# Optimization experiments

Hardware: AMD Instinct MI355X
Metric: run time of the kernel (lower is better)

## Reference

```python
import jax, jax.numpy as jnp
import numpy as np

NQ, NC, D = 100000, 2000, 128
QN, CN, MAXC = 4, 4, 4
B, S = 128, 64
HOPS, RANK_K = 2, 10


def setup_inputs() -> dict:
    key = jax.random.key(0)
    ks = jax.random.split(key, 24)
    sc = 1.0 / np.sqrt(D)
    f = lambda k, shape: (jax.random.normal(k, shape) * sc).astype(jnp.float32)
    xb = float(np.sqrt(6.0 / (B + D)))  # xavier_uniform on [B, D]
    return {
        'embed_question': f(ks[0], (NQ, D)),
        'embed_concept': f(ks[1], (NC, D)),
        'embed_correctness': f(ks[2], (2, D)),
        'W_ih1': f(ks[3], (3 * D, 2 * D)), 'W_hh1': f(ks[4], (3 * D, D)),
        'b_ih1': jnp.zeros(3 * D), 'b_hh1': jnp.zeros(3 * D),
        'W_ih2': f(ks[5], (3 * D, D)), 'W_hh2': f(ks[6], (3 * D, D)),
        'b_ih2': jnp.zeros(3 * D), 'b_hh2': jnp.zeros(3 * D),
        'W_agg': f(ks[7], (HOPS, D, D)), 'b_agg': jnp.zeros((HOPS, D)),
        'W_last': f(ks[8], (D, D)), 'b_last': jnp.zeros(D),
        'W_query': f(ks[9], (D, D)), 'b_query': jnp.zeros(D),
        'W_key': f(ks[10], (D, D)), 'b_key': jnp.zeros(D),
        'w_q': f(ks[11], (D,)), 'w_k': f(ks[12], (D,)), 'b_w': jnp.zeros(()),
        'h1_init': jax.random.uniform(ks[13], (B, D), minval=-xb, maxval=xb),
        'h2_init': jax.random.uniform(ks[14], (B, D), minval=-xb, maxval=xb),
        'question_neighbors': jax.random.randint(ks[15], (NQ, QN), 0, NC),
        'concept_neighbors': jax.random.randint(ks[16], (NC, CN), 0, NQ),
        'q2c': jax.random.randint(ks[17], (NQ, MAXC), 0, NC),
        'question_seq': jax.random.randint(ks[18], (B, S), 0, NQ),
        'correctness_seq': jax.random.randint(ks[19], (B, S), 0, 2),
        'mask_seq': jax.random.randint(ks[20], (B, S), 0, 2),
    }


def _gru(x, h, Wih, Whh, bih, bhh):
    gi = x @ Wih.T + bih
    gh = h @ Whh.T + bhh
    ir, iz, inn = jnp.split(gi, 3, axis=-1)
    hr, hz, hn = jnp.split(gh, 3, axis=-1)
    r = jax.nn.sigmoid(ir + hr)
    z = jax.nn.sigmoid(iz + hz)
    n = jnp.tanh(inn + r * hn)
    return (1.0 - z) * n + z * h


def _aggregate(embs, W_agg, b_agg, W_last, b_last):
    embs = list(embs)
    for i in range(HOPS):
        for j in range(HOPS - i):
            m = jnp.mean(embs[j + 1], axis=-2) + embs[j]
            embs[j] = jnp.tanh(m @ W_agg[j].T + b_agg[j])
    return jnp.tanh(embs[0] @ W_last.T + b_last)


def _predict(qc, states, W_query, b_query, W_key, b_key, w_q, w_k, b_w):
    # qc: [B, nqc, D]; states: [B, nst, D]
    og = jnp.einsum('bqd,bsd->bqs', qc, states)
    Qe = jnp.tanh(qc @ W_key.T + b_key)          # MLP_key(question_concepts)
    Ke = jnp.tanh(states @ W_query.T + b_query)  # MLP_query(states)
    tmp = (Qe @ w_q)[:, :, None] + (Ke @ w_k)[:, None, :] + b_w  # [B,nqc,nst]
    alpha = jax.nn.softmax(tmp, axis=2)
    return jax.nn.sigmoid(jnp.sum(alpha * og, axis=(1, 2)))


def reference(embed_question, embed_concept, embed_correctness,
              W_ih1, W_hh1, b_ih1, b_hh1, W_ih2, W_hh2, b_ih2, b_hh2,
              W_agg, b_agg, W_last, b_last, W_query, b_query, W_key, b_key,
              w_q, w_k, b_w, h1_init, h2_init,
              question_neighbors, concept_neighbors, q2c,
              question_seq, correctness_seq, mask_seq):
    h1, h2 = h1_init, h2_init
    state_history = jnp.zeros((B, S, D), jnp.float32)
    y = jnp.zeros((B, S), jnp.float32)
    for t in range(S - 1):
        q_t = question_seq[:, t]
        mask_t = mask_seq[:, t] != 0
        emb_r = embed_correctness[correctness_seq[:, t]]
        # multi-hop neighbor expansion (computed for full batch; masked rows
        # are replaced below, identical math to the original masked gather)
        nodes = [q_t]
        for i in range(HOPS):
            flat = nodes[-1].reshape(-1)
            tbl = question_neighbors if i % 2 == 0 else concept_neighbors
            nxt = tbl[flat]
            nodes.append(nxt.reshape(nodes[-1].shape + (nxt.shape[-1],)))
        embs = [embed_question[n] if i % 2 == 0 else embed_concept[n]
                for i, n in enumerate(nodes)]
        agg = _aggregate(embs, W_agg, b_agg, W_last, b_last)
        emb_q = jnp.where(mask_t[:, None], agg, embed_question[q_t])
        h1 = _gru(jnp.concatenate([emb_q, emb_r], axis=1), h1, W_ih1, W_hh1, b_ih1, b_hh1)
        g2 = _gru(h1, h2, W_ih2, W_hh2, b_ih2, b_hh2)
        q_next = question_seq[:, t + 1]
        qc = jnp.concatenate([embed_question[q_next][:, None],
                              embed_concept[q2c[q_next]]], axis=1)  # [B, 1+MAXC, D]
        if t == 0:
            y = y.at[:, 0].set(_predict(qc, g2[:, None], W_query, b_query, W_key, b_key, w_q, w_k, b_w))
            continue  # original skips h2/state_history update at t==0
        cur = g2[:, None]
        if t <= RANK_K:
            hist = jnp.concatenate([cur, state_history[:, :t]], axis=1)
        else:
            Qv = jax.lax.stop_gradient(embed_question[q_next])               # [B,D]
            Kv = jax.lax.stop_gradient(embed_question[question_seq[:, :t]])  # [B,t,D]
            scores = jnp.einsum('btd,bd->bt', Kv, Qv)
            _, idx = jax.lax.top_k(scores, RANK_K)
            sel = jnp.take_along_axis(state_history, idx[:, :, None], axis=1)
            hist = jnp.concatenate([cur, sel], axis=1)
        y = y.at[:, t + 1].set(_predict(qc, hist, W_query, b_query, W_key, b_key, w_q, w_k, b_w))
        h2 = g2
        state_history = state_history.at[:, t].set(g2)
    return y
```

## Files before the change

kernel.cpp:

```cpp
#include <hip/hip_runtime.h>
#include <math.h>

#define D    128
#define QN   4
#define CN   4
#define MAXC 4
#define BB   128
#define SS   64
#define RK   10
#define T    768

#define UOFF_IH1A 0
#define UOFF_IH1B 24576
#define UOFF_HH1  49152
#define UOFF_IH2  73728
#define UOFF_HH2  98304
#define UOFF_QRY  122880
#define UOFF_A0   131072
#define UOFF_A1   139264
#define UOFF_LS   147456
#define TOTAL_U   155648

typedef _Float16 h2_t __attribute__((ext_vector_type(2)));
union U32H2 { unsigned u; h2_t h; unsigned short s2[2]; };

__device__ __forceinline__ unsigned h16f(float x){
  U32H2 c; c.h[0] = (_Float16)x; c.h[1] = (_Float16)0.f;
  return (unsigned)c.s2[0];
}
__device__ __forceinline__ unsigned packh2(float a, float b){
  U32H2 c; c.h[0] = (_Float16)a; c.h[1] = (_Float16)b;
  return c.u;
}
__device__ __forceinline__ float dot2(unsigned w, unsigned x, float acc){
  U32H2 a; a.u = w; U32H2 b; b.u = x;
  return __builtin_amdgcn_fdot2(a.h, b.h, acc, false);
}
__device__ __forceinline__ float hlo(unsigned u){ U32H2 a; a.u=u; return (float)a.h[0]; }
__device__ __forceinline__ float hhi(unsigned u){ U32H2 a; a.u=u; return (float)a.h[1]; }

__device__ __forceinline__ float fsig(float x){ return 1.f/(1.f + __expf(-x)); }
__device__ __forceinline__ float ftanh(float x){
  float xc = fminf(fmaxf(x, -30.f), 30.f);
  float e = __expf(2.f*xc);
  return (e - 1.f)/(e + 1.f);
}

#define FD4(w4, x4, acc) { \
  acc = dot2((w4).x, (x4).x, acc); acc = dot2((w4).y, (x4).y, acc); \
  acc = dot2((w4).z, (x4).z, acc); acc = dot2((w4).w, (x4).w, acc); }

#define KEEP4(v) asm volatile("" : "+v"((v).x), "+v"((v).y), "+v"((v).z), "+v"((v).w))

__global__ void gikt_pack(const float* __restrict__ Wih1,
                          const float* __restrict__ Whh1,
                          const float* __restrict__ Wih2,
                          const float* __restrict__ Whh2,
                          const float* __restrict__ Wagg,
                          const float* __restrict__ Wlast,
                          const float* __restrict__ Wqry,
                          unsigned* __restrict__ wsU)
{
  int i = blockIdx.x * blockDim.x + threadIdx.x;
  if (i >= TOTAL_U) return;
  const float* src = nullptr; int row = 0, e2 = 0, stride = 0;
  int j = i;
  if (j < 24576) {
    int c = j & 3, i4 = j >> 2, k = i4 / 768, t = i4 - k * 768, r = t >> 1, hf = t & 1;
    e2 = hf * 32 + k * 4 + c; row = r; src = Wih1; stride = 256;
  } else if ((j -= 24576) < 24576) {
    e2 = 64 + (j / 384); row = j % 384; src = Wih1; stride = 256;
  } else if ((j -= 24576) < 24576) {
    int c = j & 3, i4 = j >> 2, k = i4 / 768, t = i4 - k * 768, r = t >> 1, hf = t & 1;
    e2 = hf * 32 + k * 4 + c; row = r; src = Whh1; stride = 128;
  } else if ((j -= 24576) < 24576) {
    int c = j & 3, i4 = j >> 2, k = i4 / 768, t = i4 - k * 768, r = t >> 1, hf = t & 1;
    e2 = hf * 32 + k * 4 + c; row = r; src = Wih2; stride = 128;
  } else if ((j -= 24576) < 24576) {
    int c = j & 3, i4 = j >> 2, k = i4 / 768, t = i4 - k * 768, r = t >> 1, hf = t & 1;
    e2 = hf * 32 + k * 4 + c; row = r; src = Whh2; stride = 128;
  } else if ((j -= 24576) < 8192) {
    int c = j & 3, i4 = j >> 2, k = i4 >> 7, r = i4 & 127;
    e2 = k * 4 + c; row = r; src = Wqry; stride = 128;
  } else if ((j -= 8192) < 8192) {
    int r = j & 127, p = (j >> 7) & 1, e2g = j >> 8;
    e2 = 2 * e2g + p; row = r; src = Wagg; stride = 128;
  } else if ((j -= 8192) < 8192) {
    int r = j & 127, p = (j >> 7) & 1, e2g = j >> 8;
    e2 = 2 * e2g + p; row = r; src = Wagg + 128 * 128; stride = 128;
  } else {
    j -= 8192;
    int r = j & 127, p = (j >> 7) & 1, e2g = j >> 8;
    e2 = 2 * e2g + p; row = r; src = Wlast; stride = 128;
  }
  float lo = src[row * stride + 2 * e2];
  float hi = src[row * stride + 2 * e2 + 1];
  wsU[i] = h16f(lo) | (h16f(hi) << 16);
}

__device__ __forceinline__ float2 gru_nl2(float2 gr, float2 gz, float2 gn,
                                          float2 hr, float2 hz, float2 hn,
                                          float2 hold){
  float2 out;
  {
    float rg = fsig(gr.x + hr.x);
    float zg = fsig(gz.x + hz.x);
    float ng = ftanh(gn.x + rg*hn.x);
    out.x = (1.f-zg)*ng + zg*hold.x;
  }
  {
    float rg = fsig(gr.y + hr.y);
    float zg = fsig(gz.y + hz.y);
    float ng = ftanh(gn.y + rg*hn.y);
    out.y = (1.f-zg)*ng + zg*hold.y;
  }
  return out;
}

__launch_bounds__(T, 1)
__global__ void gikt_main(
    const float* __restrict__ embQ,
    const float* __restrict__ embC,
    const float* __restrict__ embR,
    const float* __restrict__ b_ih1,
    const float* __restrict__ b_hh1,
    const float* __restrict__ b_ih2,
    const float* __restrict__ b_hh2,
    const float* __restrict__ b_agg,
    const float* __restrict__ b_last,
    const float* __restrict__ b_query,
    const float* __restrict__ w_k,
    const float* __restrict__ h1i,
    const float* __restrict__ h2i,
    const int* __restrict__ qnbr,
    const int* __restrict__ cnbr,
    const int* __restrict__ q2c,
    const int* __restrict__ qseq,
    const int* __restrict__ cseq,
    const int* __restrict__ mseq,
    const unsigned* __restrict__ wsU,
    float* __restrict__ y)
{
  const int b   = blockIdx.x;
  const int tid = threadIdx.x;
  const int r2  = tid >> 1, hf = tid & 1;

  __shared__ unsigned aggL[3 * 8192];
  __shared__ __align__(16) float hist[SS][132];
  __shared__ float gicorr[2][384];
  __shared__ int   idxk[SS][RK];
  __shared__ float kwh[SS];
  __shared__ __align__(16) float a_[5][D];
  __shared__ __align__(16) float gi1[3*D];
  __shared__ __align__(16) float gh1[3*D];
  __shared__ __align__(16) float gi2[3*D];
  __shared__ __align__(16) float gh2[3*D];
  __shared__ __align__(16) float h1fp[2][D];
  __shared__ __align__(16) float g2fp[2][D];
  __shared__ __align__(16) float h2ifp[D];
  __shared__ __align__(16) float qcs[2][D];
  __shared__ float kevec[D];
  __shared__ __align__(16) unsigned mPu[5][64];
  __shared__ __align__(16) unsigned vPu[64];
  __shared__ __align__(16) unsigned m1Pu[64];
  __shared__ __align__(16) unsigned xvPu[64];
  __shared__ __align__(16) unsigned h1Pu[64];
  __shared__ __align__(16) unsigned g2Pu[64];
  __shared__ __align__(16) unsigned h2iPu[64];
  __shared__ int   sq[SS], scc[SS], smk[SS];
  __shared__ int   nn1[SS][QN], nn2[SS][QN*CN], cc2[SS][MAXC];
  __shared__ float red[12];
  __shared__ float ogv[16], kwv[16];

  float (*G)[65] = (float(*)[65])aggL;

  uint4 pwi[8], pwh[8];
  {
    const uint4* Pi = (const uint4*)(wsU + UOFF_IH2);
    const uint4* Ph = (const uint4*)(wsU + UOFF_HH2);
    #pragma unroll
    for (int k = 0; k < 8; ++k) { pwi[k] = Pi[k*768 + tid]; pwh[k] = Ph[k*768 + tid]; }
    #pragma unroll
    for (int k = 0; k < 8; ++k) { KEEP4(pwi[k]); KEEP4(pwh[k]); }
  }

  for (int i = tid; i < SS; i += T) { sq[i]=qseq[b*SS+i]; scc[i]=cseq[b*SS+i]; smk[i]=mseq[b*SS+i]; }
  __syncthreads();

  for (int i = tid; i < SS*32; i += T) {
    int s = i >> 5, e4 = i & 31;
    float4 v = ((const float4*)(embQ + sq[s]*D))[e4];
    ((float4*)hist[s])[e4] = v;
  }
  for (int i = tid; i < (SS-1)*QN; i += T)   { int t = i>>2, j = i&3; nn1[t][j] = qnbr[sq[t]*QN + j]; }
  for (int i = tid; i < (SS-1)*MAXC; i += T) { int t = i>>2, j = i&3; cc2[t][j] = q2c[sq[t+1]*MAXC + j]; }
  __syncthreads();

  for (int p = tid; p < SS*SS; p += T) {
    int tq = p >> 6, s = p & 63;
    if (tq >= RK+2 && s < tq-1) {
      const float4* ra = (const float4*)hist[tq];
      const float4* rb = (const float4*)hist[s];
      float acc = 0.f;
      #pragma unroll 8
      for (int d4 = 0; d4 < 32; ++d4) {
        float4 xa = ra[d4], xb = rb[d4];
        acc += xa.x*xb.x + xa.y*xb.y + xa.z*xb.z + xa.w*xb.w;
      }
      G[tq-(RK+2)][s] = acc;
    }
  }
  for (int i = tid; i < (SS-1)*QN*CN; i += T) {
    int t = i>>4, j = (i>>2)&3, l = i&3;
    nn2[t][j*CN+l] = cnbr[nn1[t][j]*CN + l];
  }
  {
    const int c = (tid >= 384) ? 1 : 0, r = tid - (c ? 384 : 0);
    const float2* er2 = (const float2*)(embR + c*D);
    float acc = 0.f;
    #pragma unroll 4
    for (int e2l = 0; e2l < 64; ++e2l) {
      unsigned u = wsU[UOFF_IH1B + e2l*384 + r];
      float2 x = er2[e2l];
      acc += hlo(u)*x.x + hhi(u)*x.y;
    }
    gicorr[c][r] = acc;
  }
  __syncthreads();

  if (tid < 52) {
    int t = RK + 1 + tid;
    for (int k = 0; k < RK; ++k) {
      float best = -INFINITY; int bi = 0;
      for (int s = 0; s < t; ++s) { float v = G[tid][s]; if (v > best) { best = v; bi = s; } }
      idxk[t][k] = bi;
      G[tid][bi] = -INFINITY;
    }
  }
  __syncthreads();

  for (int i = tid; i < 3*8192; i += T) aggL[i] = wsU[UOFF_A0 + i];
  if (tid < 64) {
    float a0 = h1i[b*D+2*tid], a1 = h1i[b*D+2*tid+1];
    h1Pu[tid] = packh2(a0, a1);
    ((float2*)h1fp[1])[tid] = make_float2(a0, a1);
    float c0 = h2i[b*D+2*tid], c1 = h2i[b*D+2*tid+1];
    h2iPu[tid] = packh2(c0, c1);
    ((float2*)h2ifp)[tid] = make_float2(c0, c1);
    g2Pu[tid] = 0;
  }
  if (tid < D) hist[0][tid] = 0.f;
  if (tid == 0) y[b*SS + 1] = 0.f;
  {
    float p0 = (tid < D) ? w_k[tid]*ftanh(b_query[tid]) : 0.f;
    #pragma unroll
    for (int off = 32; off; off >>= 1) p0 += __shfl_down(p0, off);
    if ((tid & 63) == 0) red[tid >> 6] = p0;
  }
  __syncthreads();
  if (tid == 0) kwh[0] = red[0]+red[1];
  __syncthreads();

  const uint4* Wi1 = (const uint4*)(wsU + UOFF_IH1A);
  const uint4* Wh1 = (const uint4*)(wsU + UOFF_HH1);
  const uint4* Wq4 = (const uint4*)(wsU + UOFF_QRY);

  float pf0 = 0.f, pf1 = 0.f, pf2 = 0.f, pf3 = 0.f, pf4 = 0.f;

#define PREFETCH(tt) {                                                        \
    const int d_ = tid & 127, grp_ = tid >> 7;                                \
    const bool m2_ = (smk[tt] != 0);                                          \
    if (grp_ == 0) {                                                          \
      pf0 = embQ[sq[tt]*D + d_];                                              \
      if (m2_) { pf1 = embC[nn1[tt][0]*D+d_]; pf2 = embC[nn1[tt][1]*D+d_];    \
                 pf3 = embC[nn1[tt][2]*D+d_]; pf4 = embC[nn1[tt][3]*D+d_]; }  \
    } else if (grp_ <= 4) {                                                   \
      if (m2_) { const int j_ = grp_ - 1;                                     \
        pf0 = embC[nn1[tt][j_]*D + d_];                                       \
        pf1 = embQ[nn2[tt][j_*CN+0]*D+d_]; pf2 = embQ[nn2[tt][j_*CN+1]*D+d_]; \
        pf3 = embQ[nn2[tt][j_*CN+2]*D+d_]; pf4 = embQ[nn2[tt][j_*CN+3]*D+d_];}\
    } else {                                                                  \
      pf0 = embQ[sq[(tt)+1]*D + d_];                                          \
      pf1 = embC[cc2[tt][0]*D+d_]; pf2 = embC[cc2[tt][1]*D+d_];               \
      pf3 = embC[cc2[tt][2]*D+d_]; pf4 = embC[cc2[tt][3]*D+d_];               \
    } }

  PREFETCH(0);

  for (int t = 0; t < SS-1; ++t) {
    const int tp = t - 1;
    const bool msk = (smk[t] != 0);

    if (tid < 64 && t >= 1) {
      const int l = tid;
      const float* ph2 = (t <= 2) ? h2ifp : g2fp[t & 1];
      float2 hold = ((const float2*)ph2)[l];
      float2 gv = gru_nl2(((const float2*)gi2)[l], ((const float2*)(gi2+128))[l], ((const float2*)(gi2+256))[l],
                          ((const float2*)gh2)[l], ((const float2*)(gh2+128))[l], ((const float2*)(gh2+256))[l],
                          hold);
      ((float2*)g2fp[(t+1)&1])[l] = gv;
      g2Pu[l] = packh2(gv.x, gv.y);
      if (t >= 2) { hist[t-1][2*l] = gv.x; hist[t-1][2*l+1] = gv.y; }
    }
    {
      const int d = tid & 127, grp = tid >> 7;
      if (msk) {
        if (grp <= 4) ((_Float16*)mPu[grp])[d] = (_Float16)(pf0 + 0.25f*(pf1+pf2+pf3+pf4));
        else          qcs[t & 1][d] = pf0+pf1+pf2+pf3+pf4;
      } else {
        if (grp == 0)      ((_Float16*)xvPu)[d] = (_Float16)pf0;
        else if (grp == 5) qcs[t & 1][d] = pf0+pf1+pf2+pf3+pf4;
      }
    }
    if (t + 1 < SS-1) PREFETCH(t+1);
    __syncthreads();

    if (msk) {
      if (tid < 128) {
        const int r = tid;
        const unsigned* A = aggL;
        const uint2* x2p = (const uint2*)mPu[0];
        float acc0 = b_agg[r], acc1 = 0.f;
        #pragma unroll
        for (int e2g = 0; e2g < 32; e2g += 2) {
          unsigned u00 = A[e2g*256 + r],     u01 = A[e2g*256 + 128 + r];
          uint2 x0 = x2p[e2g];
          acc0 = dot2(u00, x0.x, acc0); acc0 = dot2(u01, x0.y, acc0);
          unsigned u10 = A[(e2g+1)*256 + r], u11 = A[(e2g+1)*256 + 128 + r];
          uint2 x1 = x2p[e2g+1];
          acc1 = dot2(u10, x1.x, acc1); acc1 = dot2(u11, x1.y, acc1);
        }
        a_[0][r] = ftanh(acc0 + acc1);
      } else if (tid < 256) {
        const int r = tid - 128;
        const unsigned* A = aggL + 8192;
        const uint2* x1p = (const uint2*)mPu[1];
        const uint2* x2p = (const uint2*)mPu[2];
        const uint2* x3p = (const uint2*)mPu[3];
        const uint2* x4p = (const uint2*)mPu[4];
        float bb = b_agg[D + r];
        float c1 = 0.f, c2 = 0.f, c3 = 0.f, c4 = 0.f;
        #pragma unroll
        for (int e2g = 0; e2g < 32; ++e2g) {
          unsigned u0 = A[e2g*256 + r], u1 = A[e2g*256 + 128 + r];
          uint2 v1 = x1p[e2g]; c1 = dot2(u0, v1.x, c1); c1 = dot2(u1, v1.y, c1);
          uint2 v2 = x2p[e2g]; c2 = dot2(u0, v2.x, c2); c2 = dot2(u1, v2.y, c2);
          uint2 v3 = x3p[e2g]; c3 = dot2(u0, v3.x, c3); c3 = dot2(u1, v3.y, c3);
          uint2 v4 = x4p[e2g]; c4 = dot2(u0, v4.x, c4); c4 = dot2(u1, v4.y, c4);
        }
        a_[1][r] = ftanh(bb + c1); a_[2][r] = ftanh(bb + c2);
        a_[3][r] = ftanh(bb + c3); a_[4][r] = ftanh(bb + c4);
      } else if (tid < 432 && t >= 1) {
        const int g = (tid - 256) >> 4, lane = tid & 15;
        const int ne = (tp < RK ? tp : RK) + 1;
        if (g < ne) {
          const float* row;
          if (g == 0) row = g2fp[(t+1)&1];
          else {
            int s = (tp <= RK) ? (g-1) : idxk[tp][g-1];
            row = hist[s];
            if (lane == 0) kwv[g] = kwh[s];
          }
          const float* qp = qcs[tp & 1];
          float part = 0.f;
          #pragma unroll
          for (int k = 0; k < 8; ++k) { int d = lane + (k<<4); part += qp[d]*row[d]; }
          part += __shfl_xor(part, 8, 16);
          part += __shfl_xor(part, 4, 16);
          part += __shfl_xor(part, 2, 16);
          part += __shfl_xor(part, 1, 16);
          if (lane == 0) ogv[g] = part;
        }
      } else if (tid >= 512) {
        const int rq = (tid - 512) >> 1, hq = tid & 1;
        const uint4* g2p4 = (const uint4*)g2Pu;
        float a0 = hq ? 0.f : b_query[rq], a1 = 0.f;
        #pragma unroll
        for (int k = hq*8; k < hq*8+8; k += 2) {
          uint4 u0 = Wq4[k*128 + rq];     uint4 x0 = g2p4[k];   FD4(u0, x0, a0);
          uint4 u1 = Wq4[(k+1)*128 + rq]; uint4 x1 = g2p4[k+1]; FD4(u1, x1, a1);
        }
        float acc = a0 + a1; acc += __shfl_xor(acc, 1);
        if (!hq) kevec[rq] = ftanh(acc) * w_k[rq];
      }
      __syncthreads();

      if (tid < 256) {
        const int l = tid & 63;
        float v0 = a_[0][2*l]   + 0.25f*(a_[1][2*l]  +a_[2][2*l]  +a_[3][2*l]  +a_[4][2*l]);
        float v1 = a_[0][2*l+1] + 0.25f*(a_[1][2*l+1]+a_[2][2*l+1]+a_[3][2*l+1]+a_[4][2*l+1]);
        vPu[l] = packh2(v0, v1);
        const int r = tid >> 1, h = tid & 1;
        const uint2* x2p = (const uint2*)vPu;
        float acc0 = h ? 0.f : b_agg[r], acc1 = 0.f;
        #pragma unroll
        for (int e2g = h*16; e2g < h*16+16; e2g += 2) {
          unsigned u00 = aggL[e2g*256 + r],     u01 = aggL[e2g*256 + 128 + r];
          uint2 x0 = x2p[e2g];
          acc0 = dot2(u00, x0.x, acc0); acc0 = dot2(u01, x0.y, acc0);
          unsigned u10 = aggL[(e2g+1)*256 + r], u11 = aggL[(e2g+1)*256 + 128 + r];
          uint2 x1 = x2p[e2g+1];
          acc1 = dot2(u10, x1.x, acc1); acc1 = dot2(u11, x1.y, acc1);
        }
        float acc = acc0 + acc1; acc += __shfl_xor(acc, 1);
        if (!h) ((_Float16*)m1Pu)[r] = (_Float16)ftanh(acc);
      } else if (tid >= 512 && tid < 576 && t >= 1) {
        const int lane = tid & 63;
        float v = kevec[lane] + kevec[lane + 64];
        #pragma unroll
        for (int off = 32; off; off >>= 1) v += __shfl_down(v, off);
        if (lane == 0) { kwv[0] = v; if (tp >= 1) kwh[tp] = v; }
      }
      __syncthreads();

      if (tid < 256) {
        const int r = tid >> 1, h = tid & 1;
        const unsigned* A = aggL + 16384;
        const uint2* x2p = (const uint2*)m1Pu;
        float acc0 = h ? 0.f : b_last[r], acc1 = 0.f;
        #pragma unroll
        for (int e2g = h*16; e2g < h*16+16; e2g += 2) {
          unsigned u00 = A[e2g*256 + r],     u01 = A[e2g*256 + 128 + r];
          uint2 x0 = x2p[e2g];
          acc0 = dot2(u00, x0.x, acc0); acc0 = dot2(u01, x0.y, acc0);
          unsigned u10 = A[(e2g+1)*256 + r], u11 = A[(e2g+1)*256 + 128 + r];
          uint2 x1 = x2p[e2g+1];
          acc1 = dot2(u10, x1.x, acc1); acc1 = dot2(u11, x1.y, acc1);
        }
        float acc = acc0 + acc1; acc += __shfl_xor(acc, 1);
        if (!h) ((_Float16*)xvPu)[r] = (_Float16)ftanh(acc);
      } else if (tid == 256 && t >= 1) {
        const int ne = (tp < RK ? tp : RK) + 1;
        float mx = kwv[0];
        for (int i2 = 1; i2 < ne; ++i2) mx = fmaxf(mx, kwv[i2]);
        float den = 0.f, num = 0.f;
        for (int i2 = 0; i2 < ne; ++i2) { float e_ = __expf(kwv[i2]-mx); den += e_; num += e_*ogv[i2]; }
        y[b*SS + ((tp==0) ? 0 : (tp+1))] = fsig(num/den);
      }
      __syncthreads();

      {
        const uint4* xvp4 = (const uint4*)xvPu;
        const uint4* h1p4 = (const uint4*)h1Pu;
        float ai0 = hf ? 0.f : (b_ih1[r2] + gicorr[scc[t]][r2]), ai1 = 0.f;
        float ah0 = hf ? 0.f : b_hh1[r2], ah1 = 0.f;
        #pragma unroll
        for (int k = 0; k < 8; k += 2) {
          uint4 w0 = Wi1[k*768 + tid], w1 = Wi1[(k+1)*768 + tid];
          uint4 xa = xvp4[hf*8+k], xb = xvp4[hf*8+k+1];
          FD4(w0, xa, ai0); FD4(w1, xb, ai1);
          uint4 v0 = Wh1[k*768 + tid], v1 = Wh1[(k+1)*768 + tid];
          uint4 ya = h1p4[hf*8+k], yb = h1p4[hf*8+k+1];
          FD4(v0, ya, ah0); FD4(v1, yb, ah1);
        }
        float acc_i = ai0 + ai1; acc_i += __shfl_xor(acc_i, 1);
        float acc_h = ah0 + ah1; acc_h += __shfl_xor(acc_h, 1);
        if (!hf) { gi1[r2] = acc_i; gh1[r2] = acc_h; }
      }
      __syncthreads();
    } else {
      if (tid >= 256 && tid < 432 && t >= 1) {
        const int g = (tid - 256) >> 4, lane = tid & 15;
        const int ne = (tp < RK ? tp : RK) + 1;
        if (g < ne) {
          const float* row;
          if (g == 0) row = g2fp[(t+1)&1];
          else {
            int s = (tp <= RK) ? (g-1) : idxk[tp][g-1];
            row = hist[s];
            if (lane == 0) kwv[g] = kwh[s];
          }
          const float* qp = qcs[tp & 1];
          float part = 0.f;
          #pragma unroll
          for (int k = 0; k < 8; ++k) { int d = lane + (k<<4); part += qp[d]*row[d]; }
          part += __shfl_xor(part, 8, 16);
          part += __shfl_xor(part, 4, 16);
          part += __shfl_xor(part, 2, 16);
          part += __shfl_xor(part, 1, 16);
          if (lane == 0) ogv[g] = part;
        }
      } else if (tid >= 512) {
        const int rq = (tid - 512) >> 1, hq = tid & 1;
        const uint4* g2p4 = (const uint4*)g2Pu;
        float a0 = hq ? 0.f : b_query[rq], a1 = 0.f;
        #pragma unroll
        for (int k = hq*8; k < hq*8+8; k += 2) {
          uint4 u0 = Wq4[k*128 + rq];     uint4 x0 = g2p4[k];   FD4(u0, x0, a0);
          uint4 u1 = Wq4[(k+1)*128 + rq]; uint4 x1 = g2p4[k+1]; FD4(u1, x1, a1);
        }
        float acc = a0 + a1; acc += __shfl_xor(acc, 1);
        if (!hq) kevec[rq] = ftanh(acc) * w_k[rq];
      }
      {
        const uint4* xvp4 = (const uint4*)xvPu;
        const uint4* h1p4 = (const uint4*)h1Pu;
        float ai0 = hf ? 0.f : (b_ih1[r2] + gicorr[scc[t]][r2]), ai1 = 0.f;
        float ah0 = hf ? 0.f : b_hh1[r2], ah1 = 0.f;
        #pragma unroll
        for (int k = 0; k < 8; k += 2) {
          uint4 w0 = Wi1[k*768 + tid], w1 = Wi1[(k+1)*768 + tid];
          uint4 xa = xvp4[hf*8+k], xb = xvp4[hf*8+k+1];
          FD4(w0, xa, ai0); FD4(w1, xb, ai1);
          uint4 v0 = Wh1[k*768 + tid], v1 = Wh1[(k+1)*768 + tid];
          uint4 ya = h1p4[hf*8+k], yb = h1p4[hf*8+k+1];
          FD4(v0, ya, ah0); FD4(v1, yb, ah1);
        }
        float acc_i = ai0 + ai1; acc_i += __shfl_xor(acc_i, 1);
        float acc_h = ah0 + ah1; acc_h += __shfl_xor(acc_h, 1);
        if (!hf) { gi1[r2] = acc_i; gh1[r2] = acc_h; }
      }
      __syncthreads();
    }

    if (!msk && t >= 1 && tid < 64) {
      float v = kevec[tid] + kevec[tid + 64];
      #pragma unroll
      for (int off = 32; off; off >>= 1) v += __shfl_down(v, off);
      if (tid == 0) {
        if (tp >= 1) kwh[tp] = v;
        const int ne = (tp < RK ? tp : RK) + 1;
        float mx = v;
        for (int i2 = 1; i2 < ne; ++i2) mx = fmaxf(mx, kwv[i2]);
        float den = __expf(v - mx), num = den*ogv[0];
        for (int i2 = 1; i2 < ne; ++i2) { float e_ = __expf(kwv[i2]-mx); den += e_; num += e_*ogv[i2]; }
        y[b*SS + ((tp==0) ? 0 : (tp+1))] = fsig(num/den);
      }
    }
    {
      const int l = tid & 63;
      float2 hold = ((const float2*)h1fp[(t+1)&1])[l];
      float2 hn = gru_nl2(((const float2*)gi1)[l], ((const float2*)(gi1+128))[l], ((const float2*)(gi1+256))[l],
                          ((const float2*)gh1)[l], ((const float2*)(gh1+128))[l], ((const float2*)(gh1+256))[l],
                          hold);
      ((float2*)h1fp[t&1])[l] = hn;
      h1Pu[l] = packh2(hn.x, hn.y);
    }
    {
      const uint4* xh1 = (const uint4*)h1Pu;
      const uint4* xh2 = (t <= 1) ? (const uint4*)h2iPu : (const uint4*)g2Pu;
      float ai0 = hf ? 0.f : b_ih2[r2], ai1 = 0.f;
      float ah0 = hf ? 0.f : b_hh2[r2], ah1 = 0.f;
      #pragma unroll
      for (int k = 0; k < 8; k += 2) {
        uint4 xa = xh1[hf*8+k], xb = xh1[hf*8+k+1];
        FD4(pwi[k], xa, ai0); FD4(pwi[k+1], xb, ai1);
        uint4 ya = xh2[hf*8+k], yb = xh2[hf*8+k+1];
        FD4(pwh[k], ya, ah0); FD4(pwh[k+1], yb, ah1);
      }
      float acc_i = ai0 + ai1; acc_i += __shfl_xor(acc_i, 1);
      float acc_h = ah0 + ah1; acc_h += __shfl_xor(acc_h, 1);
      if (!hf) { gi2[r2] = acc_i; gh2[r2] = acc_h; }
    }
    __syncthreads();
  }

  if (tid < 64) {
    const int l = tid;
    const float* ph2 = g2fp[1];
    float2 hold = ((const float2*)ph2)[l];
    float2 gv = gru_nl2(((const float2*)gi2)[l], ((const float2*)(gi2+128))[l], ((const float2*)(gi2+256))[l],
                        ((const float2*)gh2)[l], ((const float2*)(gh2+128))[l], ((const float2*)(gh2+256))[l],
                        hold);
    ((float2*)g2fp[0])[l] = gv;
    g2Pu[l] = packh2(gv.x, gv.y);
  }
  __syncthreads();
  if (tid < 128) {
    const int r = tid;
    const uint4* g2p4 = (const uint4*)g2Pu;
    float a0 = b_query[r], a1 = 0.f;
    #pragma unroll
    for (int k = 0; k < 16; k += 2) {
      uint4 u0 = Wq4[k*128 + r];     uint4 x0 = g2p4[k];   FD4(u0, x0, a0);
      uint4 u1 = Wq4[(k+1)*128 + r]; uint4 x1 = g2p4[k+1]; FD4(u1, x1, a1);
    }
    kevec[r] = ftanh(a0 + a1) * w_k[r];
  }
  __syncthreads();
  {
    const int tp = SS - 2;
    if (tid < 176) {
      const int g = tid >> 4, lane = tid & 15;
      const int ne = RK + 1;
      if (g < ne) {
        const float* row;
        if (g == 0) row = g2fp[0];
        else {
          int s = idxk[tp][g-1];
          row = hist[s];
          if (lane == 0) kwv[g] = kwh[s];
        }
        const float* qp = qcs[tp & 1];
        float part = 0.f;
        #pragma unroll
        for (int k = 0; k < 8; ++k) { int d = lane + (k<<4); part += qp[d]*row[d]; }
        part += __shfl_xor(part, 8, 16);
        part += __shfl_xor(part, 4, 16);
        part += __shfl_xor(part, 2, 16);
        part += __shfl_xor(part, 1, 16);
        if (lane == 0) ogv[g] = part;
      }
    } else if (tid >= 256 && tid < 320) {
      const int lane = tid & 63;
      float v = kevec[lane] + kevec[lane + 64];
      #pragma unroll
      for (int off = 32; off; off >>= 1) v += __shfl_down(v, off);
      if (lane == 0) kwv[0] = v;
    }
  }
  __syncthreads();
  if (tid == 0) {
    const int ne = RK + 1;
    float mx = kwv[0];
    for (int i2 = 1; i2 < ne; ++i2) mx = fmaxf(mx, kwv[i2]);
    float den = 0.f, num = 0.f;
    for (int i2 = 0; i2 < ne; ++i2) { float e_ = __expf(kwv[i2]-mx); den += e_; num += e_*ogv[i2]; }
    y[b*SS + SS - 1] = fsig(num/den);
  }
}

extern "C" void kernel_launch(void* const* d_in, const int* in_sizes, int n_in,
                              void* d_out, int out_size, void* d_ws, size_t ws_size,
                              hipStream_t stream)
{
  (void)in_sizes; (void)n_in; (void)out_size; (void)ws_size;

  const float* embQ  = (const float*)d_in[0];
  const float* embC  = (const float*)d_in[1];
  const float* embR  = (const float*)d_in[2];
  const float* Wih1  = (const float*)d_in[3];
  const float* Whh1  = (const float*)d_in[4];
  const float* bih1  = (const float*)d_in[5];
  const float* bhh1  = (const float*)d_in[6];
  const float* Wih2  = (const float*)d_in[7];
  const float* Whh2  = (const float*)d_in[8];
  const float* bih2  = (const float*)d_in[9];
  const float* bhh2  = (const float*)d_in[10];
  const float* Wagg  = (const float*)d_in[11];
  const float* bagg  = (const float*)d_in[12];
  const float* Wlast = (const float*)d_in[13];
  const float* blast = (const float*)d_in[14];
  const float* Wqry  = (const float*)d_in[15];
  const float* bqry  = (const float*)d_in[16];
  const float* wk    = (const float*)d_in[20];
  const float* h1i   = (const float*)d_in[22];
  const float* h2i   = (const float*)d_in[23];
  const int* qnbr    = (const int*)d_in[24];
  const int* cnbr    = (const int*)d_in[25];
  const int* q2c     = (const int*)d_in[26];
  const int* qseq    = (const int*)d_in[27];
  const int* cseq    = (const int*)d_in[28];
  const int* mseq    = (const int*)d_in[29];

  unsigned* wsU = (unsigned*)d_ws;
  float* yout = (float*)d_out;

  gikt_pack<<<(TOTAL_U + 255) / 256, 256, 0, stream>>>(Wih1, Whh1, Wih2, Whh2, Wagg, Wlast, Wqry, wsU);
  gikt_main<<<BB, T, 0, stream>>>(embQ, embC, embR, bih1, bhh1, bih2, bhh2, bagg, blast, bqry,
                                  wk, h1i, h2i, qnbr, cnbr, q2c, qseq, cseq, mseq, wsU, yout);
}
```

Baseline: 546.2 us.

## Pin GRU1 weights in registers and rebalance aggregation work across threads

The GRU layer-1 input and hidden weight slices are now loaded once into registers, next to the layer-2 weights, instead of being re-read from global memory every timestep. The hop-1 aggregation for the four neighbors is split across 512 threads, one neighbor each, instead of 128 threads doing all four. The query projection moves to 128 threads, one full row each, with no shuffle reduction. This cuts per-step memory traffic and shortens the critical path, at the cost of 64 more VGPRs per thread of resident weights in a 768-thread block, which risks spills.

```diff
diff --git a/kernel.cpp b/kernel.cpp
--- a/kernel.cpp
+++ b/kernel.cpp
@@ -174,14 +174,19 @@
 
   float (*G)[65] = (float(*)[65])aggL;
 
-  uint4 pwi[8], pwh[8];
+  uint4 pw1i[8], pw1h[8], pwi[8], pwh[8];
   {
+    const uint4* Pa = (const uint4*)(wsU + UOFF_IH1A);
+    const uint4* Pb = (const uint4*)(wsU + UOFF_HH1);
     const uint4* Pi = (const uint4*)(wsU + UOFF_IH2);
     const uint4* Ph = (const uint4*)(wsU + UOFF_HH2);
     #pragma unroll
-    for (int k = 0; k < 8; ++k) { pwi[k] = Pi[k*768 + tid]; pwh[k] = Ph[k*768 + tid]; }
+    for (int k = 0; k < 8; ++k) {
+      pw1i[k] = Pa[k*768 + tid]; pw1h[k] = Pb[k*768 + tid];
+      pwi[k]  = Pi[k*768 + tid]; pwh[k]  = Ph[k*768 + tid];
+    }
     #pragma unroll
-    for (int k = 0; k < 8; ++k) { KEEP4(pwi[k]); KEEP4(pwh[k]); }
+    for (int k = 0; k < 8; ++k) { KEEP4(pw1i[k]); KEEP4(pw1h[k]); KEEP4(pwi[k]); KEEP4(pwh[k]); }
   }
 
   for (int i = tid; i < SS; i += T) { sq[i]=qseq[b*SS+i]; scc[i]=cseq[b*SS+i]; smk[i]=mseq[b*SS+i]; }
@@ -261,8 +266,6 @@
   if (tid == 0) kwh[0] = red[0]+red[1];
   __syncthreads();
 
-  const uint4* Wi1 = (const uint4*)(wsU + UOFF_IH1A);
-  const uint4* Wh1 = (const uint4*)(wsU + UOFF_HH1);
   const uint4* Wq4 = (const uint4*)(wsU + UOFF_QRY);
 
   float pf0 = 0.f, pf1 = 0.f, pf2 = 0.f, pf3 = 0.f, pf4 = 0.f;
@@ -331,25 +334,53 @@
           acc1 = dot2(u10, x1.x, acc1); acc1 = dot2(u11, x1.y, acc1);
         }
         a_[0][r] = ftanh(acc0 + acc1);
-      } else if (tid < 256) {
-        const int r = tid - 128;
+      } else if (tid < 640) {
+        const int m = (tid - 128) >> 7, r = (tid - 128) & 127;
         const unsigned* A = aggL + 8192;
-        const uint2* x1p = (const uint2*)mPu[1];
-        const uint2* x2p = (const uint2*)mPu[2];
-        const uint2* x3p = (const uint2*)mPu[3];
-        const uint2* x4p = (const uint2*)mPu[4];
-        float bb = b_agg[D + r];
-        float c1 = 0.f, c2 = 0.f, c3 = 0.f, c4 = 0.f;
-        #pragma unroll
-        for (int e2g = 0; e2g < 32; ++e2g) {
-          unsigned u0 = A[e2g*256 + r], u1 = A[e2g*256 + 128 + r];
-          uint2 v1 = x1p[e2g]; c1 = dot2(u0, v1.x, c1); c1 = dot2(u1, v1.y, c1);
-          uint2 v2 = x2p[e2g]; c2 = dot2(u0, v2.x, c2); c2 = dot2(u1, v2.y, c2);
-          uint2 v3 = x3p[e2g]; c3 = dot2(u0, v3.x, c3); c3 = dot2(u1, v3.y, c3);
-          uint2 v4 = x4p[e2g]; c4 = dot2(u0, v4.x, c4); c4 = dot2(u1, v4.y, c4);
-        }
-        a_[1][r] = ftanh(bb + c1); a_[2][r] = ftanh(bb + c2);
-        a_[3][r] = ftanh(bb + c3); a_[4][r] = ftanh(bb + c4);
+        const uint2* xp = (const uint2*)mPu[1 + m];
+        float acc0 = b_agg[D + r], acc1 = 0.f;
+        #pragma unroll
+        for (int e2g = 0; e2g < 32; e2g += 2) {
+          unsigned u00 = A[e2g*256 + r],     u01 = A[e2g*256 + 128 + r];
+          uint2 x0 = xp[e2g];
+          acc0 = dot2(u00, x0.x, acc0); acc0 = dot2(u01, x0.y, acc0);
+          unsigned u10 = A[(e2g+1)*256 + r], u11 = A[(e2g+1)*256 + 128 + r];
+          uint2 x1 = xp[e2g+1];
+          acc1 = dot2(u10, x1.x, acc1); acc1 = dot2(u11, x1.y, acc1);
+        }
+        a_[1 + m][r] = ftanh(acc0 + acc1);
+      } else {
+        const int r = tid - 640;
+        const uint4* g2p4 = (const uint4*)g2Pu;
+        float a0 = b_query[r], a1 = 0.f;
+        #pragma unroll
+        for (int k = 0; k < 16; k += 2) {
+          uint4 u0 = Wq4[k*128 + r];     uint4 x0 = g2p4[k];   FD4(u0, x0, a0);
+          uint4 u1 = Wq4[(k+1)*128 + r]; uint4 x1 = g2p4[k+1]; FD4(u1, x1, a1);
+        }
+        kevec[r] = ftanh(a0 + a1) * w_k[r];
+      }
+      __syncthreads();
+
+      if (tid < 256) {
+        const int l = tid & 63;
+        float v0 = a_[0][2*l]   + 0.25f*(a_[1][2*l]  +a_[2][2*l]  +a_[3][2*l]  +a_[4][2*l]);
+        float v1 = a_[0][2*l+1] + 0.25f*(a_[1][2*l+1]+a_[2][2*l+1]+a_[3][2*l+1]+a_[4][2*l+1]);
+        vPu[l] = packh2(v0, v1);
+        const int r = tid >> 1, h = tid & 1;
+        const uint2* x2p = (const uint2*)vPu;
+        float acc0 = h ? 0.f : b_agg[r], acc1 = 0.f;
+        #pragma unroll
+        for (int e2g = h*16; e2g < h*16+16; e2g += 2) {
+          unsigned u00 = aggL[e2g*256 + r],     u01 = aggL[e2g*256 + 128 + r];
+          uint2 x0 = x2p[e2g];
+          acc0 = dot2(u00, x0.x, acc0); acc0 = dot2(u01, x0.y, acc0);
+          unsigned u10 = aggL[(e2g+1)*256 + r], u11 = aggL[(e2g+1)*256 + 128 + r];
+          uint2 x1 = x2p[e2g+1];
+          acc1 = dot2(u10, x1.x, acc1); acc1 = dot2(u11, x1.y, acc1);
+        }
+        float acc = acc0 + acc1; acc += __shfl_xor(acc, 1);
+        if (!h) ((_Float16*)m1Pu)[r] = (_Float16)ftanh(acc);
       } else if (tid < 432 && t >= 1) {
         const int g = (tid - 256) >> 4, lane = tid & 15;
         const int ne = (tp < RK ? tp : RK) + 1;
@@ -371,39 +402,6 @@
           part += __shfl_xor(part, 1, 16);
           if (lane == 0) ogv[g] = part;
         }
-      } else if (tid >= 512) {
-        const int rq = (tid - 512) >> 1, hq = tid & 1;
-        const uint4* g2p4 = (const uint4*)g2Pu;
-        float a0 = hq ? 0.f : b_query[rq], a1 = 0.f;
-        #pragma unroll
-        for (int k = hq*8; k < hq*8+8; k += 2) {
-          uint4 u0 = Wq4[k*128 + rq];     uint4 x0 = g2p4[k];   FD4(u0, x0, a0);
-          uint4 u1 = Wq4[(k+1)*128 + rq]; uint4 x1 = g2p4[k+1]; FD4(u1, x1, a1);
-        }
-        float acc = a0 + a1; acc += __shfl_xor(acc, 1);
-        if (!hq) kevec[rq] = ftanh(acc) * w_k[rq];
-      }
-      __syncthreads();
-
-      if (tid < 256) {
-        const int l = tid & 63;
-        float v0 = a_[0][2*l]   + 0.25f*(a_[1][2*l]  +a_[2][2*l]  +a_[3][2*l]  +a_[4][2*l]);
-        float v1 = a_[0][2*l+1] + 0.25f*(a_[1][2*l+1]+a_[2][2*l+1]+a_[3][2*l+1]+a_[4][2*l+1]);
-        vPu[l] = packh2(v0, v1);
-        const int r = tid >> 1, h = tid & 1;
-        const uint2* x2p = (const uint2*)vPu;
-        float acc0 = h ? 0.f : b_agg[r], acc1 = 0.f;
-        #pragma unroll
-        for (int e2g = h*16; e2g < h*16+16; e2g += 2) {
-          unsigned u00 = aggL[e2g*256 + r],     u01 = aggL[e2g*256 + 128 + r];
-          uint2 x0 = x2p[e2g];
-          acc0 = dot2(u00, x0.x, acc0); acc0 = dot2(u01, x0.y, acc0);
-          unsigned u10 = aggL[(e2g+1)*256 + r], u11 = aggL[(e2g+1)*256 + 128 + r];
-          uint2 x1 = x2p[e2g+1];
-          acc1 = dot2(u10, x1.x, acc1); acc1 = dot2(u11, x1.y, acc1);
-        }
-        float acc = acc0 + acc1; acc += __shfl_xor(acc, 1);
-        if (!h) ((_Float16*)m1Pu)[r] = (_Float16)ftanh(acc);
       } else if (tid >= 512 && tid < 576 && t >= 1) {
         const int lane = tid & 63;
         float v = kevec[lane] + kevec[lane + 64];
@@ -446,12 +444,10 @@
         float ah0 = hf ? 0.f : b_hh1[r2], ah1 = 0.f;
         #pragma unroll
         for (int k = 0; k < 8; k += 2) {
-          uint4 w0 = Wi1[k*768 + tid], w1 = Wi1[(k+1)*768 + tid];
           uint4 xa = xvp4[hf*8+k], xb = xvp4[hf*8+k+1];
-          FD4(w0, xa, ai0); FD4(w1, xb, ai1);
-          uint4 v0 = Wh1[k*768 + tid], v1 = Wh1[(k+1)*768 + tid];
+          FD4(pw1i[k], xa, ai0); FD4(pw1i[k+1], xb, ai1);
           uint4 ya = h1p4[hf*8+k], yb = h1p4[hf*8+k+1];
-          FD4(v0, ya, ah0); FD4(v1, yb, ah1);
+          FD4(pw1h[k], ya, ah0); FD4(pw1h[k+1], yb, ah1);
         }
         float acc_i = ai0 + ai1; acc_i += __shfl_xor(acc_i, 1);
         float acc_h = ah0 + ah1; acc_h += __shfl_xor(acc_h, 1);
@@ -480,17 +476,16 @@
           part += __shfl_xor(part, 1, 16);
           if (lane == 0) ogv[g] = part;
         }
-      } else if (tid >= 512) {
-        const int rq = (tid - 512) >> 1, hq = tid & 1;
+      } else if (tid >= 640) {
+        const int r = tid - 640;
         const uint4* g2p4 = (const uint4*)g2Pu;
-        float a0 = hq ? 0.f : b_query[rq], a1 = 0.f;
-        #pragma unroll
-        for (int k = hq*8; k < hq*8+8; k += 2) {
-          uint4 u0 = Wq4[k*128 + rq];     uint4 x0 = g2p4[k];   FD4(u0, x0, a0);
-          uint4 u1 = Wq4[(k+1)*128 + rq]; uint4 x1 = g2p4[k+1]; FD4(u1, x1, a1);
-        }
-        float acc = a0 + a1; acc += __shfl_xor(acc, 1);
-        if (!hq) kevec[rq] = ftanh(acc) * w_k[rq];
+        float a0 = b_query[r], a1 = 0.f;
+        #pragma unroll
+        for (int k = 0; k < 16; k += 2) {
+          uint4 u0 = Wq4[k*128 + r];     uint4 x0 = g2p4[k];   FD4(u0, x0, a0);
+          uint4 u1 = Wq4[(k+1)*128 + r]; uint4 x1 = g2p4[k+1]; FD4(u1, x1, a1);
+        }
+        kevec[r] = ftanh(a0 + a1) * w_k[r];
       }
       {
         const uint4* xvp4 = (const uint4*)xvPu;
@@ -499,12 +494,10 @@
         float ah0 = hf ? 0.f : b_hh1[r2], ah1 = 0.f;
         #pragma unroll
         for (int k = 0; k < 8; k += 2) {
-          uint4 w0 = Wi1[k*768 + tid], w1 = Wi1[(k+1)*768 + tid];
           uint4 xa = xvp4[hf*8+k], xb = xvp4[hf*8+k+1];
-          FD4(w0, xa, ai0); FD4(w1, xb, ai1);
-          uint4 v0 = Wh1[k*768 + tid], v1 = Wh1[(k+1)*768 + tid];
+          FD4(pw1i[k], xa, ai0); FD4(pw1i[k+1], xb, ai1);
           uint4 ya = h1p4[hf*8+k], yb = h1p4[hf*8+k+1];
-          FD4(v0, ya, ah0); FD4(v1, yb, ah1);
+          FD4(pw1h[k], ya, ah0); FD4(pw1h[k+1], yb, ah1);
         }
         float acc_i = ai0 + ai1; acc_i += __shfl_xor(acc_i, 1);
         float acc_h = ah0 + ah1; acc_h += __shfl_xor(acc_h, 1);
```

Result: slower. 671.6 us (+23.0%).

## Rebalance masked-step work across threads and spread hidden GRU matvec into idle phases

Applied to the files above, without the earlier changes.

In the masked branch, the four neighbour aggregation matvecs, previously done by one thread per row with four accumulators, are now spread over 512 threads with one matvec each. The query projection now uses one thread per row over 128 threads instead of two half-rows. The W_hh1·h1 gate rows are computed by threads that sat idle in the two later phases, and the final GRU phase keeps only the input-side matvec. This shortens the critical path of each serial timestep, at the cost of more thread divergence and more register pressure from the macro.

```diff
diff --git a/kernel.cpp b/kernel.cpp
--- a/kernel.cpp
+++ b/kernel.cpp
@@ -265,6 +265,16 @@
   const uint4* Wh1 = (const uint4*)(wsU + UOFF_HH1);
   const uint4* Wq4 = (const uint4*)(wsU + UOFF_QRY);
 
+#define GH1_ROW(r) {                                                   \
+    const uint4* h1p4_ = (const uint4*)h1Pu;                           \
+    float a0_ = b_hh1[r], a1_ = 0.f;                                   \
+    _Pragma("unroll")                                                  \
+    for (int k = 0; k < 8; ++k) {                                      \
+      uint4 u0_ = Wh1[k*768 + 2*(r)], u1_ = Wh1[k*768 + 2*(r) + 1];    \
+      FD4(u0_, h1p4_[k], a0_); FD4(u1_, h1p4_[8+k], a1_);              \
+    }                                                                  \
+    gh1[r] = a0_ + a1_; }
+
   float pf0 = 0.f, pf1 = 0.f, pf2 = 0.f, pf3 = 0.f, pf4 = 0.f;
 
 #define PREFETCH(tt) {                                                        \
@@ -316,11 +326,11 @@
     __syncthreads();
 
     if (msk) {
-      if (tid < 128) {
-        const int r = tid;
-        const unsigned* A = aggL;
-        const uint2* x2p = (const uint2*)mPu[0];
-        float acc0 = b_agg[r], acc1 = 0.f;
+      if (tid < 640) {
+        const int which = tid >> 7, r = tid & 127;
+        const unsigned* A = aggL + (which ? 8192 : 0);
+        const uint2* x2p = (const uint2*)mPu[which];
+        float acc0 = (which == 0) ? b_agg[r] : b_agg[D + r], acc1 = 0.f;
         #pragma unroll
         for (int e2g = 0; e2g < 32; e2g += 2) {
           unsigned u00 = A[e2g*256 + r],     u01 = A[e2g*256 + 128 + r];
@@ -330,58 +340,17 @@
           uint2 x1 = x2p[e2g+1];
           acc1 = dot2(u10, x1.x, acc1); acc1 = dot2(u11, x1.y, acc1);
         }
-        a_[0][r] = ftanh(acc0 + acc1);
-      } else if (tid < 256) {
-        const int r = tid - 128;
-        const unsigned* A = aggL + 8192;
-        const uint2* x1p = (const uint2*)mPu[1];
-        const uint2* x2p = (const uint2*)mPu[2];
-        const uint2* x3p = (const uint2*)mPu[3];
-        const uint2* x4p = (const uint2*)mPu[4];
-        float bb = b_agg[D + r];
-        float c1 = 0.f, c2 = 0.f, c3 = 0.f, c4 = 0.f;
-        #pragma unroll
-        for (int e2g = 0; e2g < 32; ++e2g) {
-          unsigned u0 = A[e2g*256 + r], u1 = A[e2g*256 + 128 + r];
-          uint2 v1 = x1p[e2g]; c1 = dot2(u0, v1.x, c1); c1 = dot2(u1, v1.y, c1);
-          uint2 v2 = x2p[e2g]; c2 = dot2(u0, v2.x, c2); c2 = dot2(u1, v2.y, c2);
-          uint2 v3 = x3p[e2g]; c3 = dot2(u0, v3.x, c3); c3 = dot2(u1, v3.y, c3);
-          uint2 v4 = x4p[e2g]; c4 = dot2(u0, v4.x, c4); c4 = dot2(u1, v4.y, c4);
-        }
-        a_[1][r] = ftanh(bb + c1); a_[2][r] = ftanh(bb + c2);
-        a_[3][r] = ftanh(bb + c3); a_[4][r] = ftanh(bb + c4);
-      } else if (tid < 432 && t >= 1) {
-        const int g = (tid - 256) >> 4, lane = tid & 15;
-        const int ne = (tp < RK ? tp : RK) + 1;
-        if (g < ne) {
-          const float* row;
-          if (g == 0) row = g2fp[(t+1)&1];
-          else {
-            int s = (tp <= RK) ? (g-1) : idxk[tp][g-1];
-            row = hist[s];
-            if (lane == 0) kwv[g] = kwh[s];
-          }
-          const float* qp = qcs[tp & 1];
-          float part = 0.f;
-          #pragma unroll
-          for (int k = 0; k < 8; ++k) { int d = lane + (k<<4); part += qp[d]*row[d]; }
-          part += __shfl_xor(part, 8, 16);
-          part += __shfl_xor(part, 4, 16);
-          part += __shfl_xor(part, 2, 16);
-          part += __shfl_xor(part, 1, 16);
-          if (lane == 0) ogv[g] = part;
-        }
-      } else if (tid >= 512) {
-        const int rq = (tid - 512) >> 1, hq = tid & 1;
+        a_[which][r] = ftanh(acc0 + acc1);
+      } else {
+        const int r = tid - 640;
         const uint4* g2p4 = (const uint4*)g2Pu;
-        float a0 = hq ? 0.f : b_query[rq], a1 = 0.f;
-        #pragma unroll
-        for (int k = hq*8; k < hq*8+8; k += 2) {
-          uint4 u0 = Wq4[k*128 + rq];     uint4 x0 = g2p4[k];   FD4(u0, x0, a0);
-          uint4 u1 = Wq4[(k+1)*128 + rq]; uint4 x1 = g2p4[k+1]; FD4(u1, x1, a1);
-        }
-        float acc = a0 + a1; acc += __shfl_xor(acc, 1);
-        if (!hq) kevec[rq] = ftanh(acc) * w_k[rq];
+        float a0 = b_query[r], a1 = 0.f;
+        #pragma unroll
+        for (int k = 0; k < 16; k += 2) {
+          uint4 u0 = Wq4[k*128 + r];     uint4 x0 = g2p4[k];   FD4(u0, x0, a0);
+          uint4 u1 = Wq4[(k+1)*128 + r]; uint4 x1 = g2p4[k+1]; FD4(u1, x1, a1);
+        }
+        kevec[r] = ftanh(a0 + a1) * w_k[r];
       }
       __syncthreads();
 
@@ -404,12 +373,43 @@
         }
         float acc = acc0 + acc1; acc += __shfl_xor(acc, 1);
         if (!h) ((_Float16*)m1Pu)[r] = (_Float16)ftanh(acc);
-      } else if (tid >= 512 && tid < 576 && t >= 1) {
-        const int lane = tid & 63;
-        float v = kevec[lane] + kevec[lane + 64];
-        #pragma unroll
-        for (int off = 32; off; off >>= 1) v += __shfl_down(v, off);
-        if (lane == 0) { kwv[0] = v; if (tp >= 1) kwh[tp] = v; }
+      } else if (tid < 432) {
+        if (t >= 1) {
+          const int g = (tid - 256) >> 4, lane = tid & 15;
+          const int ne = (tp < RK ? tp : RK) + 1;
+          if (g < ne) {
+            const float* row;
+            if (g == 0) row = g2fp[(t+1)&1];
+            else {
+              int s = (tp <= RK) ? (g-1) : idxk[tp][g-1];
+              row = hist[s];
+              if (lane == 0) kwv[g] = kwh[s];
+            }
+            const float* qp = qcs[tp & 1];
+            float part = 0.f;
+            #pragma unroll
+            for (int k = 0; k < 8; ++k) { int d = lane + (k<<4); part += qp[d]*row[d]; }
+            part += __shfl_xor(part, 8, 16);
+            part += __shfl_xor(part, 4, 16);
+            part += __shfl_xor(part, 2, 16);
+            part += __shfl_xor(part, 1, 16);
+            if (lane == 0) ogv[g] = part;
+          }
+        }
+      } else if (tid < 512) {
+        const int r = tid - 432;
+        GH1_ROW(r);
+      } else if (tid < 576) {
+        if (t >= 1) {
+          const int lane = tid & 63;
+          float v = kevec[lane] + kevec[lane + 64];
+          #pragma unroll
+          for (int off = 32; off; off >>= 1) v += __shfl_down(v, off);
+          if (lane == 0) { kwv[0] = v; if (tp >= 1) kwh[tp] = v; }
+        }
+      } else {
+        const int r = 80 + (tid - 576);
+        GH1_ROW(r);
       }
       __syncthreads();
 
@@ -429,33 +429,32 @@
         }
         float acc = acc0 + acc1; acc += __shfl_xor(acc, 1);
         if (!h) ((_Float16*)xvPu)[r] = (_Float16)ftanh(acc);
-      } else if (tid == 256 && t >= 1) {
-        const int ne = (tp < RK ? tp : RK) + 1;
-        float mx = kwv[0];
-        for (int i2 = 1; i2 < ne; ++i2) mx = fmaxf(mx, kwv[i2]);
-        float den = 0.f, num = 0.f;
-        for (int i2 = 0; i2 < ne; ++i2) { float e_ = __expf(kwv[i2]-mx); den += e_; num += e_*ogv[i2]; }
-        y[b*SS + ((tp==0) ? 0 : (tp+1))] = fsig(num/den);
+      } else if (tid == 256) {
+        if (t >= 1) {
+          const int ne = (tp < RK ? tp : RK) + 1;
+          float mx = kwv[0];
+          for (int i2 = 1; i2 < ne; ++i2) mx = fmaxf(mx, kwv[i2]);
+          float den = 0.f, num = 0.f;
+          for (int i2 = 0; i2 < ne; ++i2) { float e_ = __expf(kwv[i2]-mx); den += e_; num += e_*ogv[i2]; }
+          y[b*SS + ((tp==0) ? 0 : (tp+1))] = fsig(num/den);
+        }
+      } else if (tid >= 384 && tid < 496) {
+        const int r = 272 + (tid - 384);
+        GH1_ROW(r);
       }
       __syncthreads();
 
       {
         const uint4* xvp4 = (const uint4*)xvPu;
-        const uint4* h1p4 = (const uint4*)h1Pu;
         float ai0 = hf ? 0.f : (b_ih1[r2] + gicorr[scc[t]][r2]), ai1 = 0.f;
-        float ah0 = hf ? 0.f : b_hh1[r2], ah1 = 0.f;
         #pragma unroll
         for (int k = 0; k < 8; k += 2) {
           uint4 w0 = Wi1[k*768 + tid], w1 = Wi1[(k+1)*768 + tid];
           uint4 xa = xvp4[hf*8+k], xb = xvp4[hf*8+k+1];
           FD4(w0, xa, ai0); FD4(w1, xb, ai1);
-          uint4 v0 = Wh1[k*768 + tid], v1 = Wh1[(k+1)*768 + tid];
-          uint4 ya = h1p4[hf*8+k], yb = h1p4[hf*8+k+1];
-          FD4(v0, ya, ah0); FD4(v1, yb, ah1);
         }
         float acc_i = ai0 + ai1; acc_i += __shfl_xor(acc_i, 1);
-        float acc_h = ah0 + ah1; acc_h += __shfl_xor(acc_h, 1);
-        if (!hf) { gi1[r2] = acc_i; gh1[r2] = acc_h; }
+        if (!hf) gi1[r2] = acc_i;
       }
       __syncthreads();
     } else {
```

Measured after the change: 788.8 us. +44.4%, slower.
